# Kernel tuning notes

Hardware: AMD Instinct MI355X
Metric: run time of the kernel (lower is better)

Reference implementation:

```python
import jax, jax.numpy as jnp
import numpy as np

N = 10000
E = 330000
B = 8
F_IN = 128
UNITS = 32
H1 = 4  # gat1 heads, concat -> 128
H2 = 1  # gat2 heads, average/no-concat -> 32


def setup_inputs() -> dict:
    key = jax.random.key(0)
    ks = jax.random.split(key, 12)
    x = jax.random.normal(ks[0], (B, N, F_IN), dtype=jnp.float32)
    # edges: random src/dst plus self loops appended (as in build())
    src = jax.random.randint(ks[1], (E,), 0, N, dtype=jnp.int32)
    dst = jax.random.randint(ks[2], (E,), 0, N, dtype=jnp.int32)
    loops = jnp.arange(N, dtype=jnp.int32)
    edge_src = jnp.concatenate([src, loops])
    edge_dst = jnp.concatenate([dst, loops])
    s = 0.05
    # GAT layer 1: F_IN -> UNITS per head, H1 heads
    W1 = jax.random.normal(ks[3], (F_IN, H1, UNITS), dtype=jnp.float32) * s
    a1_src = jax.random.normal(ks[4], (H1, UNITS), dtype=jnp.float32) * s
    a1_dst = jax.random.normal(ks[5], (H1, UNITS), dtype=jnp.float32) * s
    b1 = jnp.zeros((H1 * UNITS,), dtype=jnp.float32)
    # GAT layer 2: H1*UNITS -> UNITS, 1 head
    W2 = jax.random.normal(ks[6], (H1 * UNITS, H2, UNITS), dtype=jnp.float32) * s
    a2_src = jax.random.normal(ks[7], (H2, UNITS), dtype=jnp.float32) * s
    a2_dst = jax.random.normal(ks[8], (H2, UNITS), dtype=jnp.float32) * s
    b2 = jnp.zeros((UNITS,), dtype=jnp.float32)
    return {"x": x, "edge_src": edge_src, "edge_dst": edge_dst,
            "W1": W1, "a1_src": a1_src, "a1_dst": a1_dst, "b1": b1,
            "W2": W2, "a2_src": a2_src, "a2_dst": a2_dst, "b2": b2}


def gat_conv(x, edge_src, edge_dst, W, a_src, a_dst, b, concat):
    # x: [B, N, F]; W: [F, H, U]
    Bn, Nn, _ = x.shape
    H, U = W.shape[1], W.shape[2]
    h = jnp.einsum('bnf,fhu->bnhu', x, W)  # [B,N,H,U]
    # per-node attention logits split into src/dst parts (GATv1 style)
    e_src = jnp.einsum('bnhu,hu->bnh', h, a_src)  # [B,N,H]
    e_dst = jnp.einsum('bnhu,hu->bnh', h, a_dst)
    # gather along edges; edge e: src -> dst, aggregate at dst
    logits = e_src[:, edge_src, :] + e_dst[:, edge_dst, :]  # [B,E,H]
    logits = jax.nn.leaky_relu(logits, 0.2)
    # segment softmax over incoming edges of each dst node
    seg_max = jax.ops.segment_max(jnp.moveaxis(logits, 1, 0), edge_dst,
                                  num_segments=Nn)  # [N,B,H]
    seg_max = jnp.where(jnp.isfinite(seg_max), seg_max, 0.0)
    expv = jnp.exp(jnp.moveaxis(logits, 1, 0) - seg_max[edge_dst])  # [E,B,H]
    denom = jax.ops.segment_sum(expv, edge_dst, num_segments=Nn)  # [N,B,H]
    alpha = expv / (denom[edge_dst] + 1e-9)  # [E,B,H]
    # weighted scatter-add of source features
    msg = jnp.moveaxis(h, 1, 0)[edge_src] * alpha[..., None]  # [E,B,H,U]
    out = jax.ops.segment_sum(msg, edge_dst, num_segments=Nn)  # [N,B,H,U]
    out = jnp.moveaxis(out, 0, 1)  # [B,N,H,U]
    if concat:
        out = out.reshape(Bn, Nn, H * U)
    else:
        out = out.mean(axis=2)
    return out + b


def reference(x, edge_src, edge_dst, W1, a1_src, a1_dst, b1, W2, a2_src, a2_dst, b2):
    h1 = gat_conv(x, edge_src, edge_dst, W1, a1_src, a1_dst, b1, concat=True)
    h1 = jax.nn.relu(h1)
    out = gat_conv(h1, edge_src, edge_dst, W2, a2_src, a2_dst, b2, concat=False)
    return out
```

## Files before the change

kernel.cpp:

```cpp
#include <hip/hip_runtime.h>
#include <hip/hip_fp16.h>

#define N_NODES 10000
#define BATCH 8
#define FIN 128
#define UNITS 32
#define NH1 4
#define MAXDEG 128

#define WAVE_FENCE() asm volatile("s_waitcnt lgkmcnt(0)" ::: "memory")

#define FMA_MIX_LO(acc, u, a) \
    asm("v_fma_mix_f32 %0, %1, %2, %0 op_sel:[0,0,0] op_sel_hi:[1,0,0]" \
        : "+v"(acc) : "v"(u), "v"(a))
#define FMA_MIX_HI(acc, u, a) \
    asm("v_fma_mix_f32 %0, %1, %2, %0 op_sel:[1,0,0] op_sel_hi:[1,0,0]" \
        : "+v"(acc) : "v"(u), "v"(a))

typedef _Float16 half8 __attribute__((ext_vector_type(8)));
typedef float f32x4 __attribute__((ext_vector_type(4)));

__global__ void build_prep_kernel(const int* __restrict__ esrc, const int* __restrict__ edst,
                                  int* __restrict__ deg, int* __restrict__ colPad, int E, int EB,
                                  const float* __restrict__ W1, const float* __restrict__ a1s,
                                  const float* __restrict__ a1d, const float* __restrict__ W2,
                                  const float* __restrict__ a2s, const float* __restrict__ a2d,
                                  __half* __restrict__ Wt1, __half* __restrict__ Wt2) {
    int blk = blockIdx.x;
    if (blk < EB) {
        int e = blk * 256 + threadIdx.x;
        if (e < E) {
            int d = edst[e];
            int pos = atomicAdd(&deg[d], 1);
            colPad[(d << 7) + pos] = esrc[e];
        }
        return;
    }
    int t = (blk - EB) * 256 + threadIdx.x;
    const int NP1 = 144 * 128;
    if (t < NP1) {
        int c = t >> 7, k = t & 127;
        float v = 0.f;
        if (c < 128) v = W1[k * 128 + c];
        else if (c < 132) {
            int h = c - 128;
            for (int u = 0; u < 32; ++u) v += W1[k * 128 + h * 32 + u] * a1s[h * 32 + u];
        } else if (c < 136) {
            int h = c - 132;
            for (int u = 0; u < 32; ++u) v += W1[k * 128 + h * 32 + u] * a1d[h * 32 + u];
        }
        Wt1[t] = __float2half(v);
    } else if (t < NP1 + 48 * 128) {
        int q = t - NP1;
        int c = q >> 7, k = q & 127;
        float v = 0.f;
        if (c < 32) v = W2[k * 32 + c];
        else if (c == 32) { for (int u = 0; u < 32; ++u) v += W2[k * 32 + u] * a2s[u]; }
        else if (c == 33) { for (int u = 0; u < 32; ++u) v += W2[k * 32 + u] * a2d[u]; }
        Wt2[q] = __float2half(v);
    }
}

template<typename XT, int NTILES, int HTILES, int ES>
__global__ __launch_bounds__(256)
void gemm_mfma(const XT* __restrict__ X, const __half* __restrict__ Wt,
               __half* __restrict__ Hout, float* __restrict__ es,
               float* __restrict__ ed, int rows) {
    constexpr int K = 128;
    constexpr int HCOLS = HTILES * 16;
    constexpr int PAD = 136;
    __shared__ _Float16 Wl[NTILES * 16][PAD];
    const int tid = threadIdx.x;
    for (int idx = tid; idx < NTILES * 16 * K / 8; idx += 256) {
        int r = idx >> 4, kq = idx & 15;
        *(half8*)&Wl[r][kq * 8] = *(const half8*)(Wt + r * K + kq * 8);
    }
    __syncthreads();
    const int w = tid >> 6, lane = tid & 63;
    const int row16 = blockIdx.x * 64 + w * 16;
    const int arow = row16 + (lane & 15);
    const int cl = lane & 15;
    f32x4 acc[NTILES] = {};
    #pragma unroll
    for (int kb = 0; kb < 4; ++kb) {
        int kbase = kb * 32 + ((lane >> 4) << 3);
        half8 a;
        if constexpr (sizeof(XT) == 4) {
            const float* xp = (const float*)X + (size_t)arow * K + kbase;
            float4 v0 = *(const float4*)xp;
            float4 v1 = *(const float4*)(xp + 4);
            a[0] = v0.x; a[1] = v0.y; a[2] = v0.z; a[3] = v0.w;
            a[4] = v1.x; a[5] = v1.y; a[6] = v1.z; a[7] = v1.w;
        } else {
            a = *(const half8*)((const _Float16*)X + (size_t)arow * K + kbase);
        }
        #pragma unroll
        for (int t = 0; t < NTILES; ++t) {
            half8 b = *(const half8*)&Wl[t * 16 + cl][kbase];
            acc[t] = __builtin_amdgcn_mfma_f32_16x16x32_f16(a, b, acc[t], 0, 0, 0);
        }
    }
    const int rbase = row16 + ((lane >> 4) << 2);
    #pragma unroll
    for (int t = 0; t < HTILES; ++t) {
        #pragma unroll
        for (int i = 0; i < 4; ++i)
            Hout[(size_t)(rbase + i) * HCOLS + t * 16 + cl] = __float2half(acc[t][i]);
    }
    if constexpr (ES > 0) {
        f32x4 lg = acc[HTILES];
        if (cl < ES) {
            #pragma unroll
            for (int i = 0; i < 4; ++i) es[(size_t)(rbase + i) * ES + cl] = lg[i];
        } else if (cl < 2 * ES) {
            #pragma unroll
            for (int i = 0; i < 4; ++i) ed[(size_t)(rbase + i) * ES + (cl - ES)] = lg[i];
        }
    }
}

__global__ __launch_bounds__(512)
void agg1_kernel(const int* __restrict__ deg, const int* __restrict__ colPad,
                 const float* __restrict__ es, const float* __restrict__ ed,
                 const __half* __restrict__ Hf, const float* __restrict__ bias,
                 __half* __restrict__ outH) {
    __shared__ float evS[8][MAXDEG][4];
    __shared__ int colS[8][MAXDEG];
    int blk = blockIdx.x;
    int b = blk & 7;
    int grp = blk >> 3;
    int w = threadIdx.x >> 6;
    int d = grp * 8 + w;
    int lane = threadIdx.x & 63;
    int eg = lane >> 4;
    int c8 = lane & 15;
    int head = c8 >> 2;
    int n = deg[d];
    const int* colp = colPad + (d << 7);
    size_t brow = (size_t)b * N_NODES;
    size_t drow = brow + d;
    float4 ed4 = ((const float4*)ed)[drow];
    float dx = 0.f, dy = 0.f, dz = 0.f, dw = 0.f;
    #pragma unroll
    for (int rep = 0; rep < 2; ++rep) {
        int i = lane + rep * 64;
        float4 av = make_float4(0.f, 0.f, 0.f, 0.f);
        int sv = 0;
        if (i < n) {
            sv = colp[i];
            float4 e4 = ((const float4*)es)[brow + sv];
            float l, a0, a1, a2, a3;
            l = e4.x + ed4.x; l = l > 0.f ? l : 0.2f * l; a0 = __expf(l); dx += a0;
            l = e4.y + ed4.y; l = l > 0.f ? l : 0.2f * l; a1 = __expf(l); dy += a1;
            l = e4.z + ed4.z; l = l > 0.f ? l : 0.2f * l; a2 = __expf(l); dz += a2;
            l = e4.w + ed4.w; l = l > 0.f ? l : 0.2f * l; a3 = __expf(l); dw += a3;
            av = make_float4(a0, a1, a2, a3);
        }
        *(float4*)&evS[w][i][0] = av;
        colS[w][i] = sv;
    }
    WAVE_FENCE();
    float acc[8] = {};
    const __half* hbase = Hf + (brow << 7) + (c8 << 3);
    int nR = (n + 15) & ~15;
    for (int t = 0; t < nR; t += 16) {
        int t0 = t + eg, t1 = t0 + 4, t2 = t0 + 8, t3 = t0 + 12;
        float a0 = evS[w][t0][head], a1 = evS[w][t1][head];
        float a2 = evS[w][t2][head], a3 = evS[w][t3][head];
        int s0 = colS[w][t0], s1 = colS[w][t1], s2 = colS[w][t2], s3 = colS[w][t3];
        float4 r0 = *(const float4*)(hbase + ((size_t)s0 << 7));
        float4 r1 = *(const float4*)(hbase + ((size_t)s1 << 7));
        float4 r2 = *(const float4*)(hbase + ((size_t)s2 << 7));
        float4 r3 = *(const float4*)(hbase + ((size_t)s3 << 7));
        const unsigned* u0 = (const unsigned*)&r0;
        const unsigned* u1 = (const unsigned*)&r1;
        const unsigned* u2 = (const unsigned*)&r2;
        const unsigned* u3 = (const unsigned*)&r3;
        #pragma unroll
        for (int j = 0; j < 4; ++j) {
            FMA_MIX_LO(acc[2 * j],     u0[j], a0);
            FMA_MIX_HI(acc[2 * j + 1], u0[j], a0);
        }
        #pragma unroll
        for (int j = 0; j < 4; ++j) {
            FMA_MIX_LO(acc[2 * j],     u1[j], a1);
            FMA_MIX_HI(acc[2 * j + 1], u1[j], a1);
        }
        #pragma unroll
        for (int j = 0; j < 4; ++j) {
            FMA_MIX_LO(acc[2 * j],     u2[j], a2);
            FMA_MIX_HI(acc[2 * j + 1], u2[j], a2);
        }
        #pragma unroll
        for (int j = 0; j < 4; ++j) {
            FMA_MIX_LO(acc[2 * j],     u3[j], a3);
            FMA_MIX_HI(acc[2 * j + 1], u3[j], a3);
        }
    }
    #pragma unroll
    for (int off = 32; off; off >>= 1) {
        dx += __shfl_xor(dx, off);
        dy += __shfl_xor(dy, off);
        dz += __shfl_xor(dz, off);
        dw += __shfl_xor(dw, off);
    }
    float ix = 1.f / (dx + 1e-9f);
    float iy = 1.f / (dy + 1e-9f);
    float iz = 1.f / (dz + 1e-9f);
    float iw = 1.f / (dw + 1e-9f);
    float inv = (head & 2) ? ((head & 1) ? iw : iz) : ((head & 1) ? iy : ix);
    #pragma unroll
    for (int j = 0; j < 8; ++j) {
        acc[j] += __shfl_xor(acc[j], 16);
        acc[j] += __shfl_xor(acc[j], 32);
    }
    if (eg == 0) {
        float4 b0 = *(const float4*)(bias + 8 * c8);
        float4 b1 = *(const float4*)(bias + 8 * c8 + 4);
        float vals[8];
        vals[0] = fmaxf(acc[0] * inv + b0.x, 0.f);
        vals[1] = fmaxf(acc[1] * inv + b0.y, 0.f);
        vals[2] = fmaxf(acc[2] * inv + b0.z, 0.f);
        vals[3] = fmaxf(acc[3] * inv + b0.w, 0.f);
        vals[4] = fmaxf(acc[4] * inv + b1.x, 0.f);
        vals[5] = fmaxf(acc[5] * inv + b1.y, 0.f);
        vals[6] = fmaxf(acc[6] * inv + b1.z, 0.f);
        vals[7] = fmaxf(acc[7] * inv + b1.w, 0.f);
        __half2 o[4];
        #pragma unroll
        for (int j = 0; j < 4; ++j) o[j] = __floats2half2_rn(vals[2 * j], vals[2 * j + 1]);
        *(float4*)(outH + drow * 128 + c8 * 8) = *(float4*)o;
    }
}

__global__ __launch_bounds__(512)
void agg2_kernel(const int* __restrict__ deg, const int* __restrict__ colPad,
                 const float* __restrict__ es, const float* __restrict__ ed,
                 const __half* __restrict__ Hf, const float* __restrict__ bias,
                 float* __restrict__ outF) {
    __shared__ float evS[8][MAXDEG];
    __shared__ int colS[8][MAXDEG];
    int blk = blockIdx.x;
    int b = blk & 7;
    int grp = blk >> 3;
    int w = threadIdx.x >> 6;
    int d = grp * 8 + w;
    int lane = threadIdx.x & 63;
    int eg = lane >> 2;
    int c8 = lane & 3;
    int n = deg[d];
    const int* colp = colPad + (d << 7);
    size_t brow = (size_t)b * N_NODES;
    size_t drow = brow + d;
    float edv = ed[drow];
    float den = 0.f;
    #pragma unroll
    for (int rep = 0; rep < 2; ++rep) {
        int i = lane + rep * 64;
        float av = 0.f;
        int sv = 0;
        if (i < n) {
            sv = colp[i];
            float l = es[brow + sv] + edv;
            l = l > 0.f ? l : 0.2f * l;
            av = __expf(l);
            den += av;
        }
        evS[w][i] = av;
        colS[w][i] = sv;
    }
    WAVE_FENCE();
    float acc[8] = {};
    const __half* hbase = Hf + (brow << 5) + (c8 << 3);
    int nR = (n + 31) & ~31;
    for (int t = 0; t < nR; t += 32) {
        int t0 = t + eg, t1 = t0 + 16;
        float a0 = evS[w][t0];
        float a1 = evS[w][t1];
        int s0 = colS[w][t0];
        int s1 = colS[w][t1];
        float4 r0 = *(const float4*)(hbase + ((size_t)s0 << 5));
        float4 r1 = *(const float4*)(hbase + ((size_t)s1 << 5));
        const unsigned* u0 = (const unsigned*)&r0;
        const unsigned* u1 = (const unsigned*)&r1;
        #pragma unroll
        for (int j = 0; j < 4; ++j) {
            FMA_MIX_LO(acc[2 * j],     u0[j], a0);
            FMA_MIX_HI(acc[2 * j + 1], u0[j], a0);
        }
        #pragma unroll
        for (int j = 0; j < 4; ++j) {
            FMA_MIX_LO(acc[2 * j],     u1[j], a1);
            FMA_MIX_HI(acc[2 * j + 1], u1[j], a1);
        }
    }
    #pragma unroll
    for (int off = 32; off; off >>= 1) den += __shfl_xor(den, off);
    float inv = 1.f / (den + 1e-9f);
    #pragma unroll
    for (int j = 0; j < 8; ++j) {
        acc[j] += __shfl_xor(acc[j], 4);
        acc[j] += __shfl_xor(acc[j], 8);
        acc[j] += __shfl_xor(acc[j], 16);
        acc[j] += __shfl_xor(acc[j], 32);
    }
    if (eg == 0) {
        float4 b0 = *(const float4*)(bias + 8 * c8);
        float4 b1 = *(const float4*)(bias + 8 * c8 + 4);
        float4 o0, o1;
        o0.x = acc[0] * inv + b0.x;
        o0.y = acc[1] * inv + b0.y;
        o0.z = acc[2] * inv + b0.z;
        o0.w = acc[3] * inv + b0.w;
        o1.x = acc[4] * inv + b1.x;
        o1.y = acc[5] * inv + b1.y;
        o1.z = acc[6] * inv + b1.z;
        o1.w = acc[7] * inv + b1.w;
        float* op = outF + drow * 32 + 8 * c8;
        *(float4*)op = o0;
        *(float4*)(op + 4) = o1;
    }
}

extern "C" void kernel_launch(void* const* d_in, const int* in_sizes, int n_in,
                              void* d_out, int out_size, void* d_ws, size_t ws_size,
                              hipStream_t stream) {
    const float* x    = (const float*)d_in[0];
    const int*   esrc = (const int*)d_in[1];
    const int*   edst = (const int*)d_in[2];
    const float* W1   = (const float*)d_in[3];
    const float* a1s  = (const float*)d_in[4];
    const float* a1d  = (const float*)d_in[5];
    const float* b1   = (const float*)d_in[6];
    const float* W2   = (const float*)d_in[7];
    const float* a2s  = (const float*)d_in[8];
    const float* a2d  = (const float*)d_in[9];
    const float* b2   = (const float*)d_in[10];
    float* out = (float*)d_out;
    const int E = in_sizes[1];
    const int rows = BATCH * N_NODES;

    float* wsf = (float*)d_ws;
    __half* h1h   = (__half*)wsf;
    float*  e1s   = wsf + (size_t)rows * 64;
    float*  e1d   = e1s + (size_t)rows * 4;
    __half* out1h = (__half*)(e1d + (size_t)rows * 4);
    int* deg      = (int*)((float*)out1h + (size_t)rows * 64);
    int* colPad   = deg + N_NODES;
    __half* Wt1   = (__half*)(colPad + N_NODES * 128);
    __half* Wt2   = Wt1 + 144 * 128;
    __half* h2h = h1h;
    float*  e2s = e1s;
    float*  e2d = e1s + rows;

    const int TPB = 256;
    const int EB = (E + TPB - 1) / TPB;
    const int PREPB = (144 * 128 + 48 * 128 + TPB - 1) / TPB;

    hipMemsetAsync(deg, 0, N_NODES * sizeof(int), stream);
    build_prep_kernel<<<EB + PREPB, TPB, 0, stream>>>(
        esrc, edst, deg, colPad, E, EB, W1, a1s, a1d, W2, a2s, a2d, Wt1, Wt2);

    gemm_mfma<float, 9, 8, 4><<<rows / 64, 256, 0, stream>>>(
        x, Wt1, h1h, e1s, e1d, rows);
    agg1_kernel<<<(N_NODES / 8) * BATCH, 512, 0, stream>>>(
        deg, colPad, e1s, e1d, h1h, b1, out1h);

    gemm_mfma<__half, 3, 2, 1><<<rows / 64, 256, 0, stream>>>(
        out1h, Wt2, h2h, e2s, e2d, rows);
    agg2_kernel<<<(N_NODES / 8) * BATCH, 512, 0, stream>>>(
        deg, colPad, e2s, e2d, h2h, b2, out);
}
```

Before: 149.5 us.

## Fold memset into prep kernel and run edge build alongside first GEMM

Replaces the hipMemsetAsync of the degree array with zeroing blocks inside the weight-prep kernel. The CSR-style edge bucketing (atomic degree counting and column scatter) moves out of the prep kernel into extra blocks of the first GEMM launch, so graph construction runs concurrently with the layer-1 projection. This removes one launch and lets the latency-bound atomic scatter overlap with MFMA work. In exchange, the GEMM kernel carries the build path as extra blocks, and block scheduling order now decides how well the two overlap.

```diff
diff --git a/kernel.cpp b/kernel.cpp
--- a/kernel.cpp
+++ b/kernel.cpp
@@ -20,23 +20,18 @@
 typedef _Float16 half8 __attribute__((ext_vector_type(8)));
 typedef float f32x4 __attribute__((ext_vector_type(4)));
 
-__global__ void build_prep_kernel(const int* __restrict__ esrc, const int* __restrict__ edst,
-                                  int* __restrict__ deg, int* __restrict__ colPad, int E, int EB,
-                                  const float* __restrict__ W1, const float* __restrict__ a1s,
-                                  const float* __restrict__ a1d, const float* __restrict__ W2,
-                                  const float* __restrict__ a2s, const float* __restrict__ a2d,
-                                  __half* __restrict__ Wt1, __half* __restrict__ Wt2) {
+__global__ void prep_kernel(int ZB, int* __restrict__ deg,
+                            const float* __restrict__ W1, const float* __restrict__ a1s,
+                            const float* __restrict__ a1d, const float* __restrict__ W2,
+                            const float* __restrict__ a2s, const float* __restrict__ a2d,
+                            __half* __restrict__ Wt1, __half* __restrict__ Wt2) {
     int blk = blockIdx.x;
-    if (blk < EB) {
-        int e = blk * 256 + threadIdx.x;
-        if (e < E) {
-            int d = edst[e];
-            int pos = atomicAdd(&deg[d], 1);
-            colPad[(d << 7) + pos] = esrc[e];
-        }
+    if (blk < ZB) {
+        int i = blk * 256 + threadIdx.x;
+        if (i < N_NODES) deg[i] = 0;
         return;
     }
-    int t = (blk - EB) * 256 + threadIdx.x;
+    int t = (blk - ZB) * 256 + threadIdx.x;
     const int NP1 = 144 * 128;
     if (t < NP1) {
         int c = t >> 7, k = t & 127;
@@ -62,8 +57,8 @@
 }
 
 template<typename XT, int NTILES, int HTILES, int ES>
-__global__ __launch_bounds__(256)
-void gemm_mfma(const XT* __restrict__ X, const __half* __restrict__ Wt,
+__device__ __forceinline__
+void gemm_body(int blk, const XT* __restrict__ X, const __half* __restrict__ Wt,
                __half* __restrict__ Hout, float* __restrict__ es,
                float* __restrict__ ed, int rows) {
     constexpr int K = 128;
@@ -77,7 +72,7 @@
     }
     __syncthreads();
     const int w = tid >> 6, lane = tid & 63;
-    const int row16 = blockIdx.x * 64 + w * 16;
+    const int row16 = blk * 64 + w * 16;
     const int arow = row16 + (lane & 15);
     const int cl = lane & 15;
     f32x4 acc[NTILES] = {};
@@ -117,6 +112,32 @@
             for (int i = 0; i < 4; ++i) ed[(size_t)(rbase + i) * ES + (cl - ES)] = lg[i];
         }
     }
+}
+
+__global__ __launch_bounds__(256)
+void gemm1_build(const float* __restrict__ X, const __half* __restrict__ Wt,
+                 __half* __restrict__ Hout, float* __restrict__ es,
+                 float* __restrict__ ed, int rows, int G1,
+                 const int* __restrict__ esrc, const int* __restrict__ edst,
+                 int* __restrict__ deg, int* __restrict__ colPad, int E) {
+    int blk = blockIdx.x;
+    if (blk >= G1) {
+        int e = (blk - G1) * 256 + threadIdx.x;
+        if (e < E) {
+            int d = edst[e];
+            int pos = atomicAdd(&deg[d], 1);
+            colPad[(d << 7) + pos] = esrc[e];
+        }
+        return;
+    }
+    gemm_body<float, 9, 8, 4>(blk, X, Wt, Hout, es, ed, rows);
+}
+
+__global__ __launch_bounds__(256)
+void gemm2_kernel(const __half* __restrict__ X, const __half* __restrict__ Wt,
+                  __half* __restrict__ Hout, float* __restrict__ es,
+                  float* __restrict__ ed, int rows) {
+    gemm_body<__half, 3, 2, 1>(blockIdx.x, X, Wt, Hout, es, ed, rows);
 }
 
 __global__ __launch_bounds__(512)
@@ -354,20 +375,23 @@
     float*  e2d = e1s + rows;
 
     const int TPB = 256;
+    const int ZB = (N_NODES + TPB - 1) / TPB;
+    const int PREPB = (144 * 128 + 48 * 128 + TPB - 1) / TPB;
+    const int G1 = rows / 64;
     const int EB = (E + TPB - 1) / TPB;
-    const int PREPB = (144 * 128 + 48 * 128 + TPB - 1) / TPB;
-
-    hipMemsetAsync(deg, 0, N_NODES * sizeof(int), stream);
-    build_prep_kernel<<<EB + PREPB, TPB, 0, stream>>>(
-        esrc, edst, deg, colPad, E, EB, W1, a1s, a1d, W2, a2s, a2d, Wt1, Wt2);
-
-    gemm_mfma<float, 9, 8, 4><<<rows / 64, 256, 0, stream>>>(
-        x, Wt1, h1h, e1s, e1d, rows);
+
+    prep_kernel<<<ZB + PREPB, TPB, 0, stream>>>(
+        ZB, deg, W1, a1s, a1d, W2, a2s, a2d, Wt1, Wt2);
+
+    gemm1_build<<<G1 + EB, TPB, 0, stream>>>(
+        x, Wt1, h1h, e1s, e1d, rows, G1, esrc, edst, deg, colPad, E);
+
     agg1_kernel<<<(N_NODES / 8) * BATCH, 512, 0, stream>>>(
         deg, colPad, e1s, e1d, h1h, b1, out1h);
 
-    gemm_mfma<__half, 3, 2, 1><<<rows / 64, 256, 0, stream>>>(
+    gemm2_kernel<<<rows / 64, TPB, 0, stream>>>(
         out1h, Wt2, h2h, e2s, e2d, rows);
+
     agg2_kernel<<<(N_NODES / 8) * BATCH, 512, 0, stream>>>(
         deg, colPad, e2s, e2d, h2h, b2, out);
 }
```

Measured after the change: 142.5 us. -4.7%, faster.
